# Performance work log

Hardware: AMD Instinct MI355X
Metric: run time of the kernel (lower is better)

The kernel has to match this reference:

```python
import jax, jax.numpy as jnp
import numpy as np

R = 5.0      # cutoff radius (init arg)
N = 4096     # total atoms
B = 8        # number of periodic systems in the batch


def setup_inputs() -> dict:
    key = jax.random.key(0)
    k1, k2, k3 = jax.random.split(key, 3)
    # positions in a ~20 Angstrom box (matches cell scale)
    pos = jax.random.uniform(k1, (N, 3), dtype=jnp.float32) * 20.0
    # sorted per-atom graph ids, as produced by a batched molecular loader
    batch = jnp.sort(jax.random.randint(k2, (N,), 0, B))
    # near-cubic 20A cells with small triclinic perturbation (well-conditioned)
    cell = jnp.eye(3, dtype=jnp.float32) * 20.0 + 0.5 * jax.random.normal(k3, (B, 3, 3), dtype=jnp.float32)
    return {"pos": pos, "cell": cell, "batch": batch}


def reference(pos, cell, batch):
    # Dense, fixed-shape equivalent of RadiusGraph.forward with PBC cell wrap.
    # Original returns dynamically filtered (edge_index, disp); here we return
    # the full [N,N,3] displacement grid (masked to 0 off-graph) plus the
    # boolean edge mask -- same math, jit-compatible static shapes.
    n = pos.shape[0]
    disp = pos[:, None, :] - pos[None, :, :]            # [N,N,3], row i minus col j
    # PBC minimum-image wrap: per edge, cell is taken from the ROW node's graph
    cell_n = cell[batch]                                # [N,3,3]
    inv_cellT = jnp.linalg.inv(jnp.swapaxes(cell_n, 1, 2))   # [N,3,3] = (cell^T)^{-1}
    # scaled = solve(cell^T, disp) vectorized over all pairs
    scaled = jnp.einsum('iab,ijb->ija', inv_cellT, disp)     # [N,N,3]
    disp = disp - jnp.einsum('iab,ijb->ija', cell_n, jnp.round(scaled))
    # edge validity: same graph, no self-loop, within cutoff (after wrap)
    same_graph = batch[:, None] == batch[None, :]
    not_self = ~jnp.eye(n, dtype=bool)
    mask = same_graph & not_self & (jnp.linalg.norm(disp, axis=-1) < R)
    disp = jnp.where(mask[..., None], disp, jnp.zeros((), disp.dtype))
    return disp, mask
```

## Files before the change

### kernel.cpp

```cpp
#include <hip/hip_runtime.h>
#include <math.h>

#define NATOMS 4096
#define R_CUT 5.0f
#define JPT 4
#define BLOCK 256
#define JPB (BLOCK * JPT)

__global__ __launch_bounds__(BLOCK) void radius_graph_kernel(
    const float* __restrict__ pos,
    const float* __restrict__ cell,
    const int*   __restrict__ batch,
    float* __restrict__ disp_out,
    float* __restrict__ mask_out)
{
    __shared__ float sBuf[JPB * 3];

    const int bid = blockIdx.x;
    const int i   = bid >> 2;
    const int jc  = bid & 3;
    const int tid = (int)threadIdx.x;

    const int bi = batch[i];
    const float pix = pos[i * 3 + 0];
    const float piy = pos[i * 3 + 1];
    const float piz = pos[i * 3 + 2];

    const float* C = cell + bi * 9;
    const float C00 = C[0], C01 = C[1], C02 = C[2];
    const float C10 = C[3], C11 = C[4], C12 = C[5];
    const float C20 = C[6], C21 = C[7], C22 = C[8];
    const float cof00 =  (C11 * C22 - C12 * C21);
    const float cof01 = -(C10 * C22 - C12 * C20);
    const float cof02 =  (C10 * C21 - C11 * C20);
    const float cof10 = -(C01 * C22 - C02 * C21);
    const float cof11 =  (C00 * C22 - C02 * C20);
    const float cof12 = -(C00 * C21 - C01 * C20);
    const float cof20 =  (C01 * C12 - C02 * C11);
    const float cof21 = -(C00 * C12 - C02 * C10);
    const float cof22 =  (C00 * C11 - C01 * C10);
    const float det = C00 * cof00 + C01 * cof01 + C02 * cof02;
    const float id  = 1.0f / det;
    const float A00 = cof00 * id, A01 = cof01 * id, A02 = cof02 * id;
    const float A10 = cof10 * id, A11 = cof11 * id, A12 = cof12 * id;
    const float A20 = cof20 * id, A21 = cof21 * id, A22 = cof22 * id;

    const int j0 = jc * JPB + tid * JPT;

    const float4* pj = (const float4*)(pos + (size_t)j0 * 3);
    const float4 q0 = pj[0], q1 = pj[1], q2 = pj[2];
    const int4 bj4 = *(const int4*)(batch + j0);

    const float pjx[4] = { q0.x, q0.w, q1.z, q2.y };
    const float pjy[4] = { q0.y, q1.x, q1.w, q2.z };
    const float pjz[4] = { q0.z, q1.y, q2.x, q2.w };
    const int   bj[4]  = { bj4.x, bj4.y, bj4.z, bj4.w };

    float od[12];
    float om[4];

    #pragma unroll
    for (int t = 0; t < 4; ++t) {
        const int j = j0 + t;
        const float d0 = __fsub_rn(pix, pjx[t]);
        const float d1 = __fsub_rn(piy, pjy[t]);
        const float d2 = __fsub_rn(piz, pjz[t]);

        const float s0 = __fadd_rn(__fadd_rn(__fmul_rn(A00, d0), __fmul_rn(A01, d1)), __fmul_rn(A02, d2));
        const float s1 = __fadd_rn(__fadd_rn(__fmul_rn(A10, d0), __fmul_rn(A11, d1)), __fmul_rn(A12, d2));
        const float s2 = __fadd_rn(__fadd_rn(__fmul_rn(A20, d0), __fmul_rn(A21, d1)), __fmul_rn(A22, d2));

        const float r0 = rintf(s0);
        const float r1 = rintf(s1);
        const float r2 = rintf(s2);

        const float w0 = __fsub_rn(d0, __fadd_rn(__fadd_rn(__fmul_rn(C00, r0), __fmul_rn(C01, r1)), __fmul_rn(C02, r2)));
        const float w1 = __fsub_rn(d1, __fadd_rn(__fadd_rn(__fmul_rn(C10, r0), __fmul_rn(C11, r1)), __fmul_rn(C12, r2)));
        const float w2 = __fsub_rn(d2, __fadd_rn(__fadd_rn(__fmul_rn(C20, r0), __fmul_rn(C21, r1)), __fmul_rn(C22, r2)));

        const float n2 = __fadd_rn(__fadd_rn(__fmul_rn(w0, w0), __fmul_rn(w1, w1)), __fmul_rn(w2, w2));
        const bool m = (bi == bj[t]) && (i != j) && (sqrtf(n2) < R_CUT);

        od[t * 3 + 0] = m ? w0 : 0.0f;
        od[t * 3 + 1] = m ? w1 : 0.0f;
        od[t * 3 + 2] = m ? w2 : 0.0f;
        om[t] = m ? 1.0f : 0.0f;
    }

    float4* lb = (float4*)sBuf;
    lb[tid * 3 + 0] = make_float4(od[0], od[1], od[2],  od[3]);
    lb[tid * 3 + 1] = make_float4(od[4], od[5], od[6],  od[7]);
    lb[tid * 3 + 2] = make_float4(od[8], od[9], od[10], od[11]);

    float4* mout = (float4*)(mask_out + (size_t)i * NATOMS + (size_t)jc * JPB);
    mout[tid] = make_float4(om[0], om[1], om[2], om[3]);

    __syncthreads();

    float4* gb = (float4*)(disp_out + (size_t)i * (NATOMS * 3) + (size_t)jc * (JPB * 3));
    gb[0 * BLOCK + tid] = lb[0 * BLOCK + tid];
    gb[1 * BLOCK + tid] = lb[1 * BLOCK + tid];
    gb[2 * BLOCK + tid] = lb[2 * BLOCK + tid];
}

extern "C" void kernel_launch(void* const* d_in, const int* in_sizes, int n_in,
                              void* d_out, int out_size, void* d_ws, size_t ws_size,
                              hipStream_t stream) {
    const float* pos   = (const float*)d_in[0];
    const float* cell  = (const float*)d_in[1];
    const int*   batch = (const int*)d_in[2];

    float* disp_out = (float*)d_out;
    float* mask_out = (float*)d_out + (size_t)NATOMS * NATOMS * 3;

    const int blocks = NATOMS * (NATOMS / JPB);
    radius_graph_kernel<<<blocks, BLOCK, 0, stream>>>(pos, cell, batch, disp_out, mask_out);
}
```

Before: 258.0 us.

## Memset displacement grid and scatter only in-graph within-cutoff edges

Zero-fills the whole displacement output with hipMemsetAsync, then launches one block per row atom. Each block finds that atom's graph range in the sorted batch array by binary search and computes only pairs inside that range, writing displacement values only for edges within the cutoff. The aim is to skip pair math for cross-graph pairs and rely on the memset engine for the dense zero writes. The cost is an extra memset pass over the 200MB buffer, plus scattered, uncoalesced 4-byte stores and divergent branches.

```diff
diff --git a/kernel.cpp b/kernel.cpp
--- a/kernel.cpp
+++ b/kernel.cpp
@@ -3,22 +3,29 @@
 
 #define NATOMS 4096
 #define R_CUT 5.0f
-#define JPT 4
 #define BLOCK 256
-#define JPB (BLOCK * JPT)
+#define F4_PER_ROW (NATOMS / 4)
+#define F4_PER_THREAD (F4_PER_ROW / BLOCK)
 
-__global__ __launch_bounds__(BLOCK) void radius_graph_kernel(
+__device__ __forceinline__ int lower_bound_i(const int* __restrict__ b, int n, int v) {
+    int lo = 0, hi = n;
+    while (lo < hi) { int mid = (lo + hi) >> 1; if (b[mid] < v) lo = mid + 1; else hi = mid; }
+    return lo;
+}
+__device__ __forceinline__ int upper_bound_i(const int* __restrict__ b, int n, int v) {
+    int lo = 0, hi = n;
+    while (lo < hi) { int mid = (lo + hi) >> 1; if (b[mid] <= v) lo = mid + 1; else hi = mid; }
+    return lo;
+}
+
+__global__ __launch_bounds__(BLOCK) void radius_graph_sparse_kernel(
     const float* __restrict__ pos,
     const float* __restrict__ cell,
     const int*   __restrict__ batch,
     float* __restrict__ disp_out,
     float* __restrict__ mask_out)
 {
-    __shared__ float sBuf[JPB * 3];
-
-    const int bid = blockIdx.x;
-    const int i   = bid >> 2;
-    const int jc  = bid & 3;
+    const int i   = blockIdx.x;
     const int tid = (int)threadIdx.x;
 
     const int bi = batch[i];
@@ -45,62 +52,52 @@
     const float A10 = cof10 * id, A11 = cof11 * id, A12 = cof12 * id;
     const float A20 = cof20 * id, A21 = cof21 * id, A22 = cof22 * id;
 
-    const int j0 = jc * JPB + tid * JPT;
+    const int g0 = lower_bound_i(batch, NATOMS, bi);
+    const int g1 = upper_bound_i(batch, NATOMS, bi);
 
-    const float4* pj = (const float4*)(pos + (size_t)j0 * 3);
-    const float4 q0 = pj[0], q1 = pj[1], q2 = pj[2];
-    const int4 bj4 = *(const int4*)(batch + j0);
-
-    const float pjx[4] = { q0.x, q0.w, q1.z, q2.y };
-    const float pjy[4] = { q0.y, q1.x, q1.w, q2.z };
-    const float pjz[4] = { q0.z, q1.y, q2.x, q2.w };
-    const int   bj[4]  = { bj4.x, bj4.y, bj4.z, bj4.w };
-
-    float od[12];
-    float om[4];
+    float* __restrict__ drow = disp_out + (size_t)i * (NATOMS * 3);
+    float4* __restrict__ mrow = (float4*)(mask_out + (size_t)i * NATOMS);
 
     #pragma unroll
-    for (int t = 0; t < 4; ++t) {
-        const int j = j0 + t;
-        const float d0 = __fsub_rn(pix, pjx[t]);
-        const float d1 = __fsub_rn(piy, pjy[t]);
-        const float d2 = __fsub_rn(piz, pjz[t]);
+    for (int s = 0; s < F4_PER_THREAD; ++s) {
+        const int f4 = tid + s * BLOCK;
+        const int jbase = f4 * 4;
+        float4 mv = make_float4(0.0f, 0.0f, 0.0f, 0.0f);
 
-        const float s0 = __fadd_rn(__fadd_rn(__fmul_rn(A00, d0), __fmul_rn(A01, d1)), __fmul_rn(A02, d2));
-        const float s1 = __fadd_rn(__fadd_rn(__fmul_rn(A10, d0), __fmul_rn(A11, d1)), __fmul_rn(A12, d2));
-        const float s2 = __fadd_rn(__fadd_rn(__fmul_rn(A20, d0), __fmul_rn(A21, d1)), __fmul_rn(A22, d2));
+        if (jbase + 3 >= g0 && jbase < g1) {
+            float* mvp = (float*)&mv;
+            #pragma unroll
+            for (int e = 0; e < 4; ++e) {
+                const int j = jbase + e;
+                if (j >= g0 && j < g1 && j != i) {
+                    const float d0 = __fsub_rn(pix, pos[j * 3 + 0]);
+                    const float d1 = __fsub_rn(piy, pos[j * 3 + 1]);
+                    const float d2 = __fsub_rn(piz, pos[j * 3 + 2]);
 
-        const float r0 = rintf(s0);
-        const float r1 = rintf(s1);
-        const float r2 = rintf(s2);
+                    const float s0 = __fadd_rn(__fadd_rn(__fmul_rn(A00, d0), __fmul_rn(A01, d1)), __fmul_rn(A02, d2));
+                    const float s1 = __fadd_rn(__fadd_rn(__fmul_rn(A10, d0), __fmul_rn(A11, d1)), __fmul_rn(A12, d2));
+                    const float s2 = __fadd_rn(__fadd_rn(__fmul_rn(A20, d0), __fmul_rn(A21, d1)), __fmul_rn(A22, d2));
 
-        const float w0 = __fsub_rn(d0, __fadd_rn(__fadd_rn(__fmul_rn(C00, r0), __fmul_rn(C01, r1)), __fmul_rn(C02, r2)));
-        const float w1 = __fsub_rn(d1, __fadd_rn(__fadd_rn(__fmul_rn(C10, r0), __fmul_rn(C11, r1)), __fmul_rn(C12, r2)));
-        const float w2 = __fsub_rn(d2, __fadd_rn(__fadd_rn(__fmul_rn(C20, r0), __fmul_rn(C21, r1)), __fmul_rn(C22, r2)));
+                    const float r0 = rintf(s0);
+                    const float r1 = rintf(s1);
+                    const float r2 = rintf(s2);
 
-        const float n2 = __fadd_rn(__fadd_rn(__fmul_rn(w0, w0), __fmul_rn(w1, w1)), __fmul_rn(w2, w2));
-        const bool m = (bi == bj[t]) && (i != j) && (sqrtf(n2) < R_CUT);
+                    const float w0 = __fsub_rn(d0, __fadd_rn(__fadd_rn(__fmul_rn(C00, r0), __fmul_rn(C01, r1)), __fmul_rn(C02, r2)));
+                    const float w1 = __fsub_rn(d1, __fadd_rn(__fadd_rn(__fmul_rn(C10, r0), __fmul_rn(C11, r1)), __fmul_rn(C12, r2)));
+                    const float w2 = __fsub_rn(d2, __fadd_rn(__fadd_rn(__fmul_rn(C20, r0), __fmul_rn(C21, r1)), __fmul_rn(C22, r2)));
 
-        od[t * 3 + 0] = m ? w0 : 0.0f;
-        od[t * 3 + 1] = m ? w1 : 0.0f;
-        od[t * 3 + 2] = m ? w2 : 0.0f;
-        om[t] = m ? 1.0f : 0.0f;
+                    const float n2 = __fadd_rn(__fadd_rn(__fmul_rn(w0, w0), __fmul_rn(w1, w1)), __fmul_rn(w2, w2));
+                    if (sqrtf(n2) < R_CUT) {
+                        mvp[e] = 1.0f;
+                        drow[j * 3 + 0] = w0;
+                        drow[j * 3 + 1] = w1;
+                        drow[j * 3 + 2] = w2;
+                    }
+                }
+            }
+        }
+        mrow[f4] = mv;
     }
-
-    float4* lb = (float4*)sBuf;
-    lb[tid * 3 + 0] = make_float4(od[0], od[1], od[2],  od[3]);
-    lb[tid * 3 + 1] = make_float4(od[4], od[5], od[6],  od[7]);
-    lb[tid * 3 + 2] = make_float4(od[8], od[9], od[10], od[11]);
-
-    float4* mout = (float4*)(mask_out + (size_t)i * NATOMS + (size_t)jc * JPB);
-    mout[tid] = make_float4(om[0], om[1], om[2], om[3]);
-
-    __syncthreads();
-
-    float4* gb = (float4*)(disp_out + (size_t)i * (NATOMS * 3) + (size_t)jc * (JPB * 3));
-    gb[0 * BLOCK + tid] = lb[0 * BLOCK + tid];
-    gb[1 * BLOCK + tid] = lb[1 * BLOCK + tid];
-    gb[2 * BLOCK + tid] = lb[2 * BLOCK + tid];
 }
 
 extern "C" void kernel_launch(void* const* d_in, const int* in_sizes, int n_in,
@@ -113,6 +110,8 @@
     float* disp_out = (float*)d_out;
     float* mask_out = (float*)d_out + (size_t)NATOMS * NATOMS * 3;
 
-    const int blocks = NATOMS * (NATOMS / JPB);
-    radius_graph_kernel<<<blocks, BLOCK, 0, stream>>>(pos, cell, batch, disp_out, mask_out);
+    hipMemsetAsync(disp_out, 0, (size_t)NATOMS * NATOMS * 3 * sizeof(float), stream);
+
+    radius_graph_sparse_kernel<<<NATOMS, BLOCK, 0, stream>>>(
+        pos, cell, batch, disp_out, mask_out);
 }
```

New measurement: 260.7 us. About the same (+1.0%).
